# Kernel optimization log

Measured on AMD Instinct MI355X. Metric: run time of the kernel, lower is better.

## Reference

```python
import jax, jax.numpy as jnp
import numpy as np

N_NODES = 50000
N_EDGES = 1600000
N_GRAPHS = 512
L = 3
D = 128
E_FEAT = 16
BN_EPS = 1e-5


def setup_inputs() -> dict:
    key = jax.random.key(0)
    ks = jax.random.split(key, 16)
    s = 0.05
    inp = {
        "x": jax.random.normal(ks[0], (N_NODES, D), jnp.float32),
        "edge_attr": jax.random.normal(ks[1], (N_EDGES, E_FEAT), jnp.float32),
        "el_W": jax.random.normal(ks[2], (L, E_FEAT, D), jnp.float32) * s,
        "el_b": jax.random.normal(ks[3], (L, D), jnp.float32) * s,
        "W1": jax.random.normal(ks[4], (L, D, D), jnp.float32) * s,
        "b1": jax.random.normal(ks[5], (L, D), jnp.float32) * s,
        "bn_g": jnp.ones((L, D), jnp.float32),
        "bn_b": jnp.zeros((L, D), jnp.float32),
        "bn_mean": jnp.zeros((L, D), jnp.float32),
        "bn_var": jnp.ones((L, D), jnp.float32),
        "W2": jax.random.normal(ks[6], (L, D, D), jnp.float32) * s,
        "b2": jax.random.normal(ks[7], (L, D), jnp.float32) * s,
        "lin1_W": jax.random.normal(ks[8], (L * D, L * D), jnp.float32) * s,
        "lin1_b": jax.random.normal(ks[9], (L * D,), jnp.float32) * s,
        "lin2_W": jax.random.normal(ks[10], (L * D, 1), jnp.float32) * s,
        "lin2_b": jax.random.normal(ks[11], (1,), jnp.float32) * s,
        "edge_index": jax.random.randint(ks[12], (2, N_EDGES), 0, N_NODES, jnp.int64),
        "batch": jnp.sort(jax.random.randint(ks[13], (N_NODES,), 0, N_GRAPHS, jnp.int64)),
    }
    return inp


def reference(x, edge_attr, el_W, el_b, W1, b1, bn_g, bn_b, bn_mean, bn_var,
              W2, b2, lin1_W, lin1_b, lin2_W, lin2_b, edge_index, batch):
    src, dst = edge_index[0], edge_index[1]  # x_j = x[src], aggregated into dst
    h = x
    pools = []
    for l in range(L):
        # GINEConv message: relu(x_j + Linear(edge_attr))
        e = edge_attr @ el_W[l] + el_b[l]            # [E, D]
        m = jax.nn.relu(h[src] + e)                  # [E, D]  (dominant traffic)
        aggr = jax.ops.segment_sum(m, dst, num_segments=N_NODES)  # scatter-add
        z = h + aggr                                 # (1+eps)*x_i + aggr, eps=0
        # MLP: Linear -> BatchNorm (eval) -> ReLU -> Linear
        z = z @ W1[l] + b1[l]
        z = (z - bn_mean[l]) * (bn_g[l] / jnp.sqrt(bn_var[l] + BN_EPS)) + bn_b[l]
        z = jax.nn.relu(z)
        z = z @ W2[l] + b2[l]
        h = jax.nn.relu(z)                           # outer F.relu in GINENet
        pools.append(jax.ops.segment_sum(h, batch, num_segments=N_GRAPHS))
    g = jnp.concatenate(pools, axis=1)               # [G, L*D]
    g = jax.nn.relu(g @ lin1_W + lin1_b)             # dropout inactive (eval)
    return g @ lin2_W + lin2_b                       # [G, 1]
```

## Files before the change

### kernel.cpp

```cpp
#include <hip/hip_runtime.h>

#define N_NODES   50000
#define N_EDGES   1600000
#define N_GRAPHS  512
#define LAYERS    3
#define D         128
#define EF        16
#define BN_EPS    1e-5f

#define SCAN_CH   256
#define SCAN_NB   ((N_NODES + SCAN_CH - 1) / SCAN_CH)

typedef _Float16 half2v __attribute__((ext_vector_type(2)));
typedef short bf16x8 __attribute__((ext_vector_type(8)));
typedef float f32x4 __attribute__((ext_vector_type(4)));

__device__ __forceinline__ float fdot2h(unsigned a, half2v b, float c) {
#if __has_builtin(__builtin_amdgcn_fdot2)
    return __builtin_amdgcn_fdot2(__builtin_bit_cast(half2v, a), b, c, false);
#else
    half2v av = __builtin_bit_cast(half2v, a);
    return fmaf((float)av[0], (float)b[0], fmaf((float)av[1], (float)b[1], c));
#endif
}

__device__ __forceinline__ unsigned pack_h2(float x, float y) {
    half2v t; t[0] = (_Float16)x; t[1] = (_Float16)y;
    return __builtin_bit_cast(unsigned, t);
}

__device__ __forceinline__ unsigned short f2bf(float f) {
    unsigned u = __builtin_bit_cast(unsigned, f);
    u += 0x7FFF + ((u >> 16) & 1);
    return (unsigned short)(u >> 16);
}

__device__ __forceinline__ float bf2f(unsigned short u) {
    return __builtin_bit_cast(float, (unsigned)u << 16);
}

__global__ __launch_bounds__(256) void hist_kernel(
    const int* __restrict__ dst, int* __restrict__ counts)
{
    int e = blockIdx.x * 256 + threadIdx.x;
    atomicAdd(&counts[dst[e]], 1);
}

__global__ __launch_bounds__(256) void scan1_kernel(
    const int* __restrict__ counts, int* __restrict__ blocksum)
{
    const int t = threadIdx.x;
    const int i = blockIdx.x * SCAN_CH + t;
    int v = (i < N_NODES) ? counts[i] : 0;
    #pragma unroll
    for (int off = 32; off > 0; off >>= 1)
        v += __shfl_down(v, off);
    __shared__ int ws[4];
    if ((t & 63) == 0) ws[t >> 6] = v;
    __syncthreads();
    if (t == 0) blocksum[blockIdx.x] = ws[0] + ws[1] + ws[2] + ws[3];
}

__global__ __launch_bounds__(256) void scan2_kernel(
    const int* __restrict__ blocksum, int* __restrict__ blockbase)
{
    __shared__ int s[256];
    const int t = threadIdx.x;
    int v = (t < SCAN_NB) ? blocksum[t] : 0;
    s[t] = v;
    __syncthreads();
    for (int off = 1; off < 256; off <<= 1) {
        int u = (t >= off) ? s[t - off] : 0;
        __syncthreads();
        s[t] += u;
        __syncthreads();
    }
    if (t < SCAN_NB) blockbase[t] = s[t] - v;
}

__global__ __launch_bounds__(256) void scan3_kernel(
    const int* __restrict__ counts, const int* __restrict__ blockbase,
    int* __restrict__ offsets, int* __restrict__ cursor)
{
    __shared__ int s[256];
    const int t = threadIdx.x;
    const int i = blockIdx.x * SCAN_CH + t;
    int v = (i < N_NODES) ? counts[i] : 0;
    s[t] = v;
    __syncthreads();
    for (int off = 1; off < 256; off <<= 1) {
        int u = (t >= off) ? s[t - off] : 0;
        __syncthreads();
        s[t] += u;
        __syncthreads();
    }
    if (i < N_NODES) {
        const int base = blockbase[blockIdx.x];
        const int excl = base + s[t] - v;
        offsets[i] = excl;
        cursor[i]  = excl;
        if (i == N_NODES - 1) offsets[N_NODES] = base + s[t];
    }
}

__global__ __launch_bounds__(256) void scatter_kernel(
    const int* __restrict__ src, const int* __restrict__ dst,
    const float* __restrict__ edge_attr,
    int* __restrict__ cursor, int* __restrict__ sorted_src,
    uint4* __restrict__ sorted_eah)
{
    int e = blockIdx.x * 256 + threadIdx.x;
    int d = dst[e];
    int pos = atomicAdd(&cursor[d], 1);
    sorted_src[pos] = src[e];
    const float4* ea = (const float4*)(edge_attr + (size_t)e * EF);
    float4 a0 = ea[0], a1 = ea[1], a2 = ea[2], a3 = ea[3];
    uint4 o0, o1;
    o0.x = pack_h2(a0.x, a0.y); o0.y = pack_h2(a0.z, a0.w);
    o0.z = pack_h2(a1.x, a1.y); o0.w = pack_h2(a1.z, a1.w);
    o1.x = pack_h2(a2.x, a2.y); o1.y = pack_h2(a2.z, a2.w);
    o1.z = pack_h2(a3.x, a3.y); o1.w = pack_h2(a3.z, a3.w);
    sorted_eah[(size_t)pos * 2]     = o0;
    sorted_eah[(size_t)pos * 2 + 1] = o1;
}

__global__ __launch_bounds__(512) void goff_kernel(
    const int* __restrict__ batch, int* __restrict__ goff)
{
    const int g = threadIdx.x;
    int lo = 0, hi = N_NODES;
    while (lo < hi) {
        int mid = (lo + hi) >> 1;
        if (batch[mid] < g) lo = mid + 1; else hi = mid;
    }
    goff[g] = lo;
    if (g == 0) goff[N_GRAPHS] = N_NODES;
}

__global__ __launch_bounds__(256) void wprep_kernel(
    const float* __restrict__ W1, const float* __restrict__ W2,
    unsigned short* __restrict__ Wt)
{
    const int matid = blockIdx.x;
    const int l = matid >> 1;
    const float* srcm = (matid & 1) ? (W2 + (size_t)l * D * D)
                                    : (W1 + (size_t)l * D * D);
    unsigned short* out = Wt + (size_t)matid * D * D;
    for (int i = 0; i < 64; ++i) {
        int idx = threadIdx.x + i * 256;
        int k = idx >> 7, n = idx & 127;
        out[n * D + k] = f2bf(srcm[idx]);
    }
}

__global__ __launch_bounds__(256) void xprep_kernel(
    const float* __restrict__ x, unsigned short* __restrict__ xb)
{
    int i = blockIdx.x * 256 + threadIdx.x;
    xb[i] = f2bf(x[i]);
}

__global__ __launch_bounds__(128) void aggr_kernel(
    const unsigned short* __restrict__ h_b,
    const uint4* __restrict__ sorted_ea,
    const int*   __restrict__ sorted_src,
    const int*   __restrict__ offsets,
    const float* __restrict__ elW,
    const float* __restrict__ elb,
    unsigned* __restrict__ zin_b)
{
    const int lane = threadIdx.x & 63;
    const int wv   = __builtin_amdgcn_readfirstlane(threadIdx.x >> 6);
    const int n    = blockIdx.x;
    const int j0   = lane * 2;

    half2v wA[8], wB[8];
    #pragma unroll
    for (int k = 0; k < 8; ++k) {
        half2v ta, tb;
        ta[0] = (_Float16)elW[(2*k    ) * D + j0];
        ta[1] = (_Float16)elW[(2*k + 1) * D + j0];
        tb[0] = (_Float16)elW[(2*k    ) * D + j0 + 1];
        tb[1] = (_Float16)elW[(2*k + 1) * D + j0 + 1];
        wA[k] = ta; wB[k] = tb;
    }
    const float biasA = elb[j0];
    const float biasB = elb[j0 + 1];

    const int beg = offsets[n];
    const int end = offsets[n + 1];
    const int cnt = end - beg;
    const int h0  = (cnt + 1) >> 1;
    const int lo  = wv ? beg + h0 : beg;
    const int hi  = wv ? end : beg + h0;

    float accA = 0.0f, accB = 0.0f;
    #pragma unroll 2
    for (int e = lo; e < hi; ++e) {
        const uint4 p0 = sorted_ea[(size_t)e * 2];
        const uint4 p1 = sorted_ea[(size_t)e * 2 + 1];
        const int   s  = sorted_src[e];
        const unsigned hv2 = *(const unsigned*)(h_b + (size_t)s * D + j0);
        float dA = biasA, dB = biasB;
        dA = fdot2h(p0.x, wA[0], dA);  dB = fdot2h(p0.x, wB[0], dB);
        dA = fdot2h(p0.y, wA[1], dA);  dB = fdot2h(p0.y, wB[1], dB);
        dA = fdot2h(p0.z, wA[2], dA);  dB = fdot2h(p0.z, wB[2], dB);
        dA = fdot2h(p0.w, wA[3], dA);  dB = fdot2h(p0.w, wB[3], dB);
        dA = fdot2h(p1.x, wA[4], dA);  dB = fdot2h(p1.x, wB[4], dB);
        dA = fdot2h(p1.y, wA[5], dA);  dB = fdot2h(p1.y, wB[5], dB);
        dA = fdot2h(p1.z, wA[6], dA);  dB = fdot2h(p1.z, wB[6], dB);
        dA = fdot2h(p1.w, wA[7], dA);  dB = fdot2h(p1.w, wB[7], dB);
        const float hA = __builtin_bit_cast(float, hv2 << 16);
        const float hB = __builtin_bit_cast(float, hv2 & 0xFFFF0000u);
        accA += fmaxf(hA + dA, 0.0f);
        accB += fmaxf(hB + dB, 0.0f);
    }

    __shared__ float2 part2[64];
    if (wv == 1) part2[lane] = make_float2(accA, accB);
    __syncthreads();
    if (wv == 0) {
        float2 p = part2[lane];
        const unsigned hs2 = *(const unsigned*)(h_b + (size_t)n * D + j0);
        const float hA = __builtin_bit_cast(float, hs2 << 16);
        const float hB = __builtin_bit_cast(float, hs2 & 0xFFFF0000u);
        const float a = hA + accA + p.x;
        const float b = hB + accB + p.y;
        zin_b[(size_t)n * 64 + lane] =
            ((unsigned)f2bf(a)) | ((unsigned)f2bf(b) << 16);
    }
}

__global__ __launch_bounds__(128) void node_mlp(
    const unsigned short* __restrict__ zin_b,
    const unsigned short* __restrict__ W1t,
    const float* __restrict__ b1,
    const float* __restrict__ bng, const float* __restrict__ bnb,
    const float* __restrict__ bnm, const float* __restrict__ bnv,
    const unsigned short* __restrict__ W2t,
    const float* __restrict__ b2,
    unsigned short* __restrict__ hout_b)
{
    __shared__ unsigned short zmid[64 * 136];
    __shared__ float scale_s[128], shift_s[128], b2_s[128];

    const int tid  = threadIdx.x;
    const int wv   = tid >> 6;
    const int lane = tid & 63;
    const int q    = lane >> 4;
    const int m    = lane & 15;
    const int node0 = blockIdx.x * 64;

    {
        float sc = bng[tid] * rsqrtf(bnv[tid] + BN_EPS);
        scale_s[tid] = sc;
        shift_s[tid] = b1[tid] * sc + bnb[tid] - bnm[tid] * sc;
        b2_s[tid]    = b2[tid];
    }

    bf16x8 a[2][4];
    #pragma unroll
    for (int sub = 0; sub < 2; ++sub) {
        int node = node0 + wv * 32 + sub * 16 + m;
        if (node >= N_NODES) node = N_NODES - 1;
        const uint4* zrow = (const uint4*)(zin_b + (size_t)node * D);
        #pragma unroll
        for (int k = 0; k < 4; ++k)
            a[sub][k] = __builtin_bit_cast(bf16x8, zrow[k * 4 + q]);
    }

    f32x4 acc[2][8];
    #pragma unroll
    for (int s2 = 0; s2 < 2; ++s2)
        #pragma unroll
        for (int t = 0; t < 8; ++t)
            acc[s2][t] = (f32x4){0.f, 0.f, 0.f, 0.f};

    __syncthreads();

    #pragma unroll
    for (int t = 0; t < 8; ++t) {
        const unsigned short* wrow = W1t + (size_t)(t * 16 + m) * D;
        bf16x8 bfr[4];
        #pragma unroll
        for (int k = 0; k < 4; ++k)
            bfr[k] = __builtin_bit_cast(bf16x8, *(const uint4*)&wrow[k * 32 + q * 8]);
        #pragma unroll
        for (int sub = 0; sub < 2; ++sub) {
            acc[sub][t] = __builtin_amdgcn_mfma_f32_16x16x32_bf16(a[sub][0], bfr[0], acc[sub][t], 0, 0, 0);
            acc[sub][t] = __builtin_amdgcn_mfma_f32_16x16x32_bf16(a[sub][1], bfr[1], acc[sub][t], 0, 0, 0);
            acc[sub][t] = __builtin_amdgcn_mfma_f32_16x16x32_bf16(a[sub][2], bfr[2], acc[sub][t], 0, 0, 0);
            acc[sub][t] = __builtin_amdgcn_mfma_f32_16x16x32_bf16(a[sub][3], bfr[3], acc[sub][t], 0, 0, 0);
        }
    }

    #pragma unroll
    for (int sub = 0; sub < 2; ++sub)
        #pragma unroll
        for (int t = 0; t < 8; ++t) {
            int col = t * 16 + m;
            float sc = scale_s[col], sh = shift_s[col];
            #pragma unroll
            for (int rr = 0; rr < 4; ++rr) {
                float v = fmaxf(acc[sub][t][rr] * sc + sh, 0.f);
                int row = wv * 32 + sub * 16 + q * 4 + rr;
                zmid[row * 136 + col] = f2bf(v);
            }
        }

    __syncthreads();

    bf16x8 a2[2][4];
    #pragma unroll
    for (int sub = 0; sub < 2; ++sub) {
        const unsigned short* zr = &zmid[(wv * 32 + sub * 16 + m) * 136];
        #pragma unroll
        for (int k = 0; k < 4; ++k)
            a2[sub][k] = __builtin_bit_cast(bf16x8, *(const uint4*)&zr[k * 32 + q * 8]);
    }

    #pragma unroll
    for (int s2 = 0; s2 < 2; ++s2)
        #pragma unroll
        for (int t = 0; t < 8; ++t)
            acc[s2][t] = (f32x4){0.f, 0.f, 0.f, 0.f};

    #pragma unroll
    for (int t = 0; t < 8; ++t) {
        const unsigned short* wrow = W2t + (size_t)(t * 16 + m) * D;
        bf16x8 bfr[4];
        #pragma unroll
        for (int k = 0; k < 4; ++k)
            bfr[k] = __builtin_bit_cast(bf16x8, *(const uint4*)&wrow[k * 32 + q * 8]);
        #pragma unroll
        for (int sub = 0; sub < 2; ++sub) {
            acc[sub][t] = __builtin_amdgcn_mfma_f32_16x16x32_bf16(a2[sub][0], bfr[0], acc[sub][t], 0, 0, 0);
            acc[sub][t] = __builtin_amdgcn_mfma_f32_16x16x32_bf16(a2[sub][1], bfr[1], acc[sub][t], 0, 0, 0);
            acc[sub][t] = __builtin_amdgcn_mfma_f32_16x16x32_bf16(a2[sub][2], bfr[2], acc[sub][t], 0, 0, 0);
            acc[sub][t] = __builtin_amdgcn_mfma_f32_16x16x32_bf16(a2[sub][3], bfr[3], acc[sub][t], 0, 0, 0);
        }
    }

    #pragma unroll
    for (int sub = 0; sub < 2; ++sub)
        #pragma unroll
        for (int rr = 0; rr < 4; ++rr) {
            int node = node0 + wv * 32 + sub * 16 + q * 4 + rr;
            if (node < N_NODES) {
                unsigned short* hrow = hout_b + (size_t)node * D;
                #pragma unroll
                for (int t = 0; t < 8; ++t) {
                    int col = t * 16 + m;
                    hrow[col] = f2bf(fmaxf(acc[sub][t][rr] + b2_s[col], 0.f));
                }
            }
        }
}

__global__ __launch_bounds__(512) void pool_kernel(
    const unsigned short* __restrict__ hout_b, const int* __restrict__ goff,
    float* __restrict__ pool, int layer_off)
{
    __shared__ float part[3][128];
    const int g = blockIdx.x;
    const int j = threadIdx.x & 127;
    const int grp = threadIdx.x >> 7;
    const int beg = goff[g], end = goff[g + 1];
    const int len = end - beg;
    const int ch  = (len + 3) >> 2;
    int lo = beg + grp * ch;
    int hi = lo + ch;
    if (hi > end) hi = end;
    float acc = 0.0f;
    for (int r = lo; r < hi; ++r)
        acc += bf2f(hout_b[(size_t)r * D + j]);
    if (grp) part[grp - 1][j] = acc;
    __syncthreads();
    if (grp == 0)
        pool[g * (LAYERS * D) + layer_off + j] =
            acc + part[0][j] + part[1][j] + part[2][j];
}

__global__ __launch_bounds__(384) void head_kernel(
    const float* __restrict__ pool,
    const float* __restrict__ lin1W,
    const float* __restrict__ lin1b,
    const float* __restrict__ lin2W,
    const float* __restrict__ lin2b,
    float*       __restrict__ out)
{
    __shared__ float gs[LAYERS * D];
    __shared__ float red[LAYERS * D];
    const int g   = blockIdx.x;
    const int tid = threadIdx.x;
    gs[tid] = pool[g * (LAYERS * D) + tid];
    __syncthreads();

    float acc = lin1b[tid];
    #pragma unroll 4
    for (int k = 0; k < LAYERS * D; ++k)
        acc = fmaf(gs[k], lin1W[k * (LAYERS * D) + tid], acc);
    acc = fmaxf(acc, 0.0f);
    float p = acc * lin2W[tid];

    red[tid] = p;
    __syncthreads();
    if (tid < 128) red[tid] = red[tid] + red[tid + 128] + red[tid + 256];
    __syncthreads();
    if (tid < 64) {
        float v = red[tid] + red[tid + 64];
        v += __shfl_down(v, 32);
        v += __shfl_down(v, 16);
        v += __shfl_down(v, 8);
        v += __shfl_down(v, 4);
        v += __shfl_down(v, 2);
        v += __shfl_down(v, 1);
        if (tid == 0) out[g] = v + lin2b[0];
    }
}

extern "C" void kernel_launch(void* const* d_in, const int* in_sizes, int n_in,
                              void* d_out, int out_size, void* d_ws, size_t ws_size,
                              hipStream_t stream)
{
    const float* x         = (const float*)d_in[0];
    const float* edge_attr = (const float*)d_in[1];
    const float* elW       = (const float*)d_in[2];
    const float* elb       = (const float*)d_in[3];
    const float* W1        = (const float*)d_in[4];
    const float* b1        = (const float*)d_in[5];
    const float* bn_g      = (const float*)d_in[6];
    const float* bn_b      = (const float*)d_in[7];
    const float* bn_mean   = (const float*)d_in[8];
    const float* bn_var    = (const float*)d_in[9];
    const float* W2        = (const float*)d_in[10];
    const float* b2        = (const float*)d_in[11];
    const float* lin1W     = (const float*)d_in[12];
    const float* lin1b     = (const float*)d_in[13];
    const float* lin2W     = (const float*)d_in[14];
    const float* lin2b     = (const float*)d_in[15];
    const int*   ei        = (const int*)d_in[16];
    const int*   batch     = (const int*)d_in[17];
    const int*   src = ei;
    const int*   dst = ei + N_EDGES;

    float*          pool       = (float*)d_ws;
    unsigned short* xb         = (unsigned short*)(pool + (size_t)N_GRAPHS * LAYERS * D);
    unsigned short* hA_b       = xb   + (size_t)N_NODES * D;
    unsigned short* zin_b      = hA_b + (size_t)N_NODES * D;
    unsigned short* Wt         = zin_b + (size_t)N_NODES * D;
    unsigned*       sorted_eah = (unsigned*)(Wt + 6 * D * D);
    int*            sorted_src = (int*)(sorted_eah + (size_t)N_EDGES * 8);
    int*            counts     = sorted_src + N_EDGES;
    int*            offsets    = counts + N_NODES;
    int*            cursor     = offsets + N_NODES + 4;
    int*            goff       = cursor + N_NODES + 4;
    int*            blocksum   = goff + N_GRAPHS + 4;
    int*            blockbase  = blocksum + SCAN_NB + 4;

    hipMemsetAsync(counts, 0, (size_t)N_NODES * sizeof(int), stream);

    wprep_kernel<<<6, 256, 0, stream>>>(W1, W2, Wt);
    xprep_kernel<<<(N_NODES * D) / 256, 256, 0, stream>>>(x, xb);
    goff_kernel<<<1, 512, 0, stream>>>(batch, goff);
    hist_kernel<<<N_EDGES / 256, 256, 0, stream>>>(dst, counts);
    scan1_kernel<<<SCAN_NB, 256, 0, stream>>>(counts, blocksum);
    scan2_kernel<<<1, 256, 0, stream>>>(blocksum, blockbase);
    scan3_kernel<<<SCAN_NB, 256, 0, stream>>>(counts, blockbase, offsets, cursor);
    scatter_kernel<<<N_EDGES / 256, 256, 0, stream>>>(
        src, dst, edge_attr, cursor, sorted_src, (uint4*)sorted_eah);

    const unsigned short* hin_b = xb;
    for (int l = 0; l < LAYERS; ++l) {
        aggr_kernel<<<N_NODES, 128, 0, stream>>>(
            hin_b, (const uint4*)sorted_eah, sorted_src, offsets,
            elW + (size_t)l * EF * D, elb + l * D, (unsigned*)zin_b);
        node_mlp<<<(N_NODES + 63) / 64, 128, 0, stream>>>(
            zin_b,
            Wt + (size_t)(l * 2)     * D * D, b1 + l * D,
            bn_g + l * D, bn_b + l * D, bn_mean + l * D, bn_var + l * D,
            Wt + (size_t)(l * 2 + 1) * D * D, b2 + l * D,
            hA_b);
        pool_kernel<<<N_GRAPHS, 512, 0, stream>>>(hA_b, goff, pool, l * D);
        hin_b = hA_b;
    }

    head_kernel<<<N_GRAPHS, LAYERS * D, 0, stream>>>(
        pool, lin1W, lin1b, lin2W, lin2b, (float*)d_out);
}
```

Measured before the change: 820.1 us.

## Compute edge-linear projection in aggregation with bf16 MFMA over 16-edge chunks

The per-edge edge_attr @ el_W projection in the aggregation kernel now runs as a 16x16x32 bf16 MFMA over chunks of 16 edges, replacing per-lane fdot2 half-precision loops. The bias is folded in through a constant-1 column in the A fragment. Edge attributes are stored as bf16 instead of fp16, and the weights are pre-packed into MFMA B fragments by a new prep kernel. Padding edges point to a dummy node row filled with large negative bf16 values, so ReLU zeroes them out. This trades scalar dot-product ALU work for matrix-core work, but the gathers of h become strided 2-byte loads, which may hurt memory efficiency, and bf16 edge attributes lose precision.

```diff
diff --git a/kernel.cpp b/kernel.cpp
--- a/kernel.cpp
+++ b/kernel.cpp
@@ -11,23 +11,9 @@
 #define SCAN_CH   256
 #define SCAN_NB   ((N_NODES + SCAN_CH - 1) / SCAN_CH)
 
-typedef _Float16 half2v __attribute__((ext_vector_type(2)));
+typedef unsigned int u32;
 typedef short bf16x8 __attribute__((ext_vector_type(8)));
 typedef float f32x4 __attribute__((ext_vector_type(4)));
-
-__device__ __forceinline__ float fdot2h(unsigned a, half2v b, float c) {
-#if __has_builtin(__builtin_amdgcn_fdot2)
-    return __builtin_amdgcn_fdot2(__builtin_bit_cast(half2v, a), b, c, false);
-#else
-    half2v av = __builtin_bit_cast(half2v, a);
-    return fmaf((float)av[0], (float)b[0], fmaf((float)av[1], (float)b[1], c));
-#endif
-}
-
-__device__ __forceinline__ unsigned pack_h2(float x, float y) {
-    half2v t; t[0] = (_Float16)x; t[1] = (_Float16)y;
-    return __builtin_bit_cast(unsigned, t);
-}
 
 __device__ __forceinline__ unsigned short f2bf(float f) {
     unsigned u = __builtin_bit_cast(unsigned, f);
@@ -37,6 +23,10 @@
 
 __device__ __forceinline__ float bf2f(unsigned short u) {
     return __builtin_bit_cast(float, (unsigned)u << 16);
+}
+
+__device__ __forceinline__ u32 pack_bf2(float x, float y) {
+    return ((u32)f2bf(x)) | ((u32)f2bf(y) << 16);
 }
 
 __global__ __launch_bounds__(256) void hist_kernel(
@@ -116,18 +106,23 @@
     const float4* ea = (const float4*)(edge_attr + (size_t)e * EF);
     float4 a0 = ea[0], a1 = ea[1], a2 = ea[2], a3 = ea[3];
     uint4 o0, o1;
-    o0.x = pack_h2(a0.x, a0.y); o0.y = pack_h2(a0.z, a0.w);
-    o0.z = pack_h2(a1.x, a1.y); o0.w = pack_h2(a1.z, a1.w);
-    o1.x = pack_h2(a2.x, a2.y); o1.y = pack_h2(a2.z, a2.w);
-    o1.z = pack_h2(a3.x, a3.y); o1.w = pack_h2(a3.z, a3.w);
+    o0.x = pack_bf2(a0.x, a0.y); o0.y = pack_bf2(a0.z, a0.w);
+    o0.z = pack_bf2(a1.x, a1.y); o0.w = pack_bf2(a1.z, a1.w);
+    o1.x = pack_bf2(a2.x, a2.y); o1.y = pack_bf2(a2.z, a2.w);
+    o1.z = pack_bf2(a3.x, a3.y); o1.w = pack_bf2(a3.z, a3.w);
     sorted_eah[(size_t)pos * 2]     = o0;
     sorted_eah[(size_t)pos * 2 + 1] = o1;
 }
 
 __global__ __launch_bounds__(512) void goff_kernel(
-    const int* __restrict__ batch, int* __restrict__ goff)
+    const int* __restrict__ batch, int* __restrict__ goff,
+    u32* __restrict__ xb_dummy, u32* __restrict__ hA_dummy)
 {
     const int g = threadIdx.x;
+    if (g < 64) {
+        xb_dummy[g] = 0xFF7FFF7Fu;
+        hA_dummy[g] = 0xFF7FFF7Fu;
+    }
     int lo = 0, hi = N_NODES;
     while (lo < hi) {
         int mid = (lo + hi) >> 1;
@@ -153,6 +148,32 @@
     }
 }
 
+__global__ __launch_bounds__(512) void elprep_kernel(
+    const float* __restrict__ elW, const float* __restrict__ elb,
+    uint4* __restrict__ elWf)
+{
+    const int l    = blockIdx.x;
+    const int t    = threadIdx.x >> 6;
+    const int lane = threadIdx.x & 63;
+    const int q = lane >> 4, c = lane & 15;
+    const float* W = elW + (size_t)l * EF * D;
+    unsigned short h[8];
+    #pragma unroll
+    for (int i = 0; i < 8; ++i) {
+        int k = q * 8 + i;
+        float v = 0.f;
+        if (q < 2)                 v = W[k * D + t * 16 + c];
+        else if (q == 2 && i == 0) v = elb[l * D + t * 16 + c];
+        h[i] = f2bf(v);
+    }
+    uint4 o;
+    o.x = (u32)h[0] | ((u32)h[1] << 16);
+    o.y = (u32)h[2] | ((u32)h[3] << 16);
+    o.z = (u32)h[4] | ((u32)h[5] << 16);
+    o.w = (u32)h[6] | ((u32)h[7] << 16);
+    elWf[((size_t)l * 8 + t) * 64 + lane] = o;
+}
+
 __global__ __launch_bounds__(256) void xprep_kernel(
     const float* __restrict__ x, unsigned short* __restrict__ xb)
 {
@@ -165,69 +186,101 @@
     const uint4* __restrict__ sorted_ea,
     const int*   __restrict__ sorted_src,
     const int*   __restrict__ offsets,
-    const float* __restrict__ elW,
-    const float* __restrict__ elb,
-    unsigned* __restrict__ zin_b)
-{
-    const int lane = threadIdx.x & 63;
-    const int wv   = __builtin_amdgcn_readfirstlane(threadIdx.x >> 6);
+    const uint4* __restrict__ elWf,
+    u32* __restrict__ zin_b)
+{
+    const int tid  = threadIdx.x;
+    const int wv   = tid >> 6;
+    const int lane = tid & 63;
+    const int q    = lane >> 4;
+    const int c    = lane & 15;
     const int n    = blockIdx.x;
-    const int j0   = lane * 2;
-
-    half2v wA[8], wB[8];
-    #pragma unroll
-    for (int k = 0; k < 8; ++k) {
-        half2v ta, tb;
-        ta[0] = (_Float16)elW[(2*k    ) * D + j0];
-        ta[1] = (_Float16)elW[(2*k + 1) * D + j0];
-        tb[0] = (_Float16)elW[(2*k    ) * D + j0 + 1];
-        tb[1] = (_Float16)elW[(2*k + 1) * D + j0 + 1];
-        wA[k] = ta; wB[k] = tb;
-    }
-    const float biasA = elb[j0];
-    const float biasB = elb[j0 + 1];
+
+    bf16x8 bfr[8];
+    #pragma unroll
+    for (int t = 0; t < 8; ++t)
+        bfr[t] = __builtin_bit_cast(bf16x8, elWf[t * 64 + lane]);
+
+    const u32 mand = (q < 2) ? 0xFFFFFFFFu : 0u;
+    const u32 mor0 = (q == 2) ? 0x3F80u : 0u;
 
     const int beg = offsets[n];
     const int end = offsets[n + 1];
-    const int cnt = end - beg;
-    const int h0  = (cnt + 1) >> 1;
-    const int lo  = wv ? beg + h0 : beg;
-    const int hi  = wv ? end : beg + h0;
-
-    float accA = 0.0f, accB = 0.0f;
-    #pragma unroll 2
-    for (int e = lo; e < hi; ++e) {
-        const uint4 p0 = sorted_ea[(size_t)e * 2];
-        const uint4 p1 = sorted_ea[(size_t)e * 2 + 1];
-        const int   s  = sorted_src[e];
-        const unsigned hv2 = *(const unsigned*)(h_b + (size_t)s * D + j0);
-        float dA = biasA, dB = biasB;
-        dA = fdot2h(p0.x, wA[0], dA);  dB = fdot2h(p0.x, wB[0], dB);
-        dA = fdot2h(p0.y, wA[1], dA);  dB = fdot2h(p0.y, wB[1], dB);
-        dA = fdot2h(p0.z, wA[2], dA);  dB = fdot2h(p0.z, wB[2], dB);
-        dA = fdot2h(p0.w, wA[3], dA);  dB = fdot2h(p0.w, wB[3], dB);
-        dA = fdot2h(p1.x, wA[4], dA);  dB = fdot2h(p1.x, wB[4], dB);
-        dA = fdot2h(p1.y, wA[5], dA);  dB = fdot2h(p1.y, wB[5], dB);
-        dA = fdot2h(p1.z, wA[6], dA);  dB = fdot2h(p1.z, wB[6], dB);
-        dA = fdot2h(p1.w, wA[7], dA);  dB = fdot2h(p1.w, wB[7], dB);
-        const float hA = __builtin_bit_cast(float, hv2 << 16);
-        const float hB = __builtin_bit_cast(float, hv2 & 0xFFFF0000u);
-        accA += fmaxf(hA + dA, 0.0f);
-        accB += fmaxf(hB + dB, 0.0f);
-    }
-
-    __shared__ float2 part2[64];
-    if (wv == 1) part2[lane] = make_float2(accA, accB);
-    __syncthreads();
+    const int nch = (end - beg + 15) >> 4;
+
+    float acc[8];
+    #pragma unroll
+    for (int t = 0; t < 8; ++t) acc[t] = 0.f;
+
+    const f32x4 zero4 = (f32x4){0.f, 0.f, 0.f, 0.f};
+
+    for (int ch = wv; ch < nch; ch += 2) {
+        const int e0 = beg + ch * 16;
+
+        uint4 araw = sorted_ea[(size_t)(e0 + c) * 2 + (q & 1)];
+        uint4 aw;
+        aw.x = (araw.x & mand) | mor0;
+        aw.y =  araw.y & mand;
+        aw.z =  araw.z & mand;
+        aw.w =  araw.w & mand;
+        const bf16x8 afr = __builtin_bit_cast(bf16x8, aw);
+
+        const int er0 = e0 + q * 4;
+        int s0 = (er0 + 0 < end) ? sorted_src[er0 + 0] : N_NODES;
+        int s1 = (er0 + 1 < end) ? sorted_src[er0 + 1] : N_NODES;
+        int s2 = (er0 + 2 < end) ? sorted_src[er0 + 2] : N_NODES;
+        int s3 = (er0 + 3 < end) ? sorted_src[er0 + 3] : N_NODES;
+        const unsigned short* hr0 = h_b + (size_t)s0 * D + c;
+        const unsigned short* hr1 = h_b + (size_t)s1 * D + c;
+        const unsigned short* hr2 = h_b + (size_t)s2 * D + c;
+        const unsigned short* hr3 = h_b + (size_t)s3 * D + c;
+
+        unsigned short hv0[8], hv1[8], hv2[8], hv3[8];
+        #pragma unroll
+        for (int t = 0; t < 8; ++t) {
+            hv0[t] = hr0[t * 16];
+            hv1[t] = hr1[t * 16];
+            hv2[t] = hr2[t * 16];
+            hv3[t] = hr3[t * 16];
+        }
+
+        #pragma unroll
+        for (int t = 0; t < 8; ++t) {
+            f32x4 C = __builtin_amdgcn_mfma_f32_16x16x32_bf16(
+                afr, bfr[t], zero4, 0, 0, 0);
+            float v0 = fmaxf(C[0] + bf2f(hv0[t]), 0.f);
+            float v1 = fmaxf(C[1] + bf2f(hv1[t]), 0.f);
+            float v2 = fmaxf(C[2] + bf2f(hv2[t]), 0.f);
+            float v3 = fmaxf(C[3] + bf2f(hv3[t]), 0.f);
+            acc[t] += (v0 + v1) + (v2 + v3);
+        }
+    }
+
+    #pragma unroll
+    for (int t = 0; t < 8; ++t) {
+        float v = acc[t];
+        v += __shfl_xor(v, 16);
+        v += __shfl_xor(v, 32);
+        acc[t] = v;
+    }
+
+    __shared__ float sums[2][128];
+    if (lane < 32) {
+        const int tb = (lane >> 4) * 4;
+        #pragma unroll
+        for (int j = 0; j < 4; ++j)
+            sums[wv][(tb + j) * 16 + c] = acc[tb + j];
+    }
+    __syncthreads();
+
     if (wv == 0) {
-        float2 p = part2[lane];
-        const unsigned hs2 = *(const unsigned*)(h_b + (size_t)n * D + j0);
+        float2 r0 = ((const float2*)sums[0])[lane];
+        float2 r1 = ((const float2*)sums[1])[lane];
+        const u32 hs2 = *(const u32*)(h_b + (size_t)n * D + 2 * lane);
         const float hA = __builtin_bit_cast(float, hs2 << 16);
         const float hB = __builtin_bit_cast(float, hs2 & 0xFFFF0000u);
-        const float a = hA + accA + p.x;
-        const float b = hB + accB + p.y;
         zin_b[(size_t)n * 64 + lane] =
-            ((unsigned)f2bf(a)) | ((unsigned)f2bf(b) << 16);
+            pack_bf2(hA + r0.x + r1.x, hB + r0.y + r1.y);
     }
 }
 
@@ -446,12 +499,13 @@
 
     float*          pool       = (float*)d_ws;
     unsigned short* xb         = (unsigned short*)(pool + (size_t)N_GRAPHS * LAYERS * D);
-    unsigned short* hA_b       = xb   + (size_t)N_NODES * D;
-    unsigned short* zin_b      = hA_b + (size_t)N_NODES * D;
+    unsigned short* hA_b       = xb   + (size_t)(N_NODES + 1) * D;
+    unsigned short* zin_b      = hA_b + (size_t)(N_NODES + 1) * D;
     unsigned short* Wt         = zin_b + (size_t)N_NODES * D;
-    unsigned*       sorted_eah = (unsigned*)(Wt + 6 * D * D);
-    int*            sorted_src = (int*)(sorted_eah + (size_t)N_EDGES * 8);
-    int*            counts     = sorted_src + N_EDGES;
+    uint4*          elWf       = (uint4*)(Wt + 6 * D * D);
+    u32*            sorted_eah = (u32*)(elWf + LAYERS * 8 * 64);
+    int*            sorted_src = (int*)(sorted_eah + (size_t)(N_EDGES + 16) * 8);
+    int*            counts     = sorted_src + N_EDGES + 16;
     int*            offsets    = counts + N_NODES;
     int*            cursor     = offsets + N_NODES + 4;
     int*            goff       = cursor + N_NODES + 4;
@@ -459,10 +513,14 @@
     int*            blockbase  = blocksum + SCAN_NB + 4;
 
     hipMemsetAsync(counts, 0, (size_t)N_NODES * sizeof(int), stream);
+    hipMemsetAsync(sorted_eah + (size_t)N_EDGES * 8, 0, 16 * 32, stream);
+    hipMemsetAsync(sorted_src + N_EDGES, 0, 16 * sizeof(int), stream);
 
     wprep_kernel<<<6, 256, 0, stream>>>(W1, W2, Wt);
+    elprep_kernel<<<LAYERS, 512, 0, stream>>>(elW, elb, elWf);
     xprep_kernel<<<(N_NODES * D) / 256, 256, 0, stream>>>(x, xb);
-    goff_kernel<<<1, 512, 0, stream>>>(batch, goff);
+    goff_kernel<<<1, 512, 0, stream>>>(batch, goff,
+        (u32*)(xb + (size_t)N_NODES * D), (u32*)(hA_b + (size_t)N_NODES * D));
     hist_kernel<<<N_EDGES / 256, 256, 0, stream>>>(dst, counts);
     scan1_kernel<<<SCAN_NB, 256, 0, stream>>>(counts, blocksum);
     scan2_kernel<<<1, 256, 0, stream>>>(blocksum, blockbase);
@@ -474,7 +532,7 @@
     for (int l = 0; l < LAYERS; ++l) {
         aggr_kernel<<<N_NODES, 128, 0, stream>>>(
             hin_b, (const uint4*)sorted_eah, sorted_src, offsets,
-            elW + (size_t)l * EF * D, elb + l * D, (unsigned*)zin_b);
+            elWf + (size_t)l * 8 * 64, (u32*)zin_b);
         node_mlp<<<(N_NODES + 63) / 64, 128, 0, stream>>>(
             zin_b,
             Wt + (size_t)(l * 2)     * D * D, b1 + l * D,
```

Result: slower. 869.1 us (+6.0%).
